# Optimization experiments

Hardware: AMD Instinct MI355X
Metric: run time of the kernel (lower is better)

Reference implementation:

```python
import jax, jax.numpy as jnp
import numpy as np

RBF_DIM = 64          # args.radius_emb_dim
FOLD_DIM = 128        # args.fold_dim
PROT_RADIUS = 30.0    # args.protein_radius (GaussianSmearing stop)
NP_, NL_, E_ = 100000, 50000, 500000


def gaussian_smearing(d):
    # GaussianSmearing(start=0, stop=PROT_RADIUS, num_gaussians=RBF_DIM)
    offsets = jnp.linspace(0.0, PROT_RADIUS, RBF_DIM, dtype=d.dtype)  # [R]
    coeff = -0.5 / (offsets[1] - offsets[0]) ** 2
    return jnp.exp(coeff * (d[:, None] - offsets[None, :]) ** 2)  # [E, R]


def setup_inputs() -> dict:
    key = jax.random.key(0)
    ks = jax.random.split(key, 12)
    scale = 10.0  # spread positions so distances span [0, PROT_RADIUS]
    pos = lambda k, n: jax.random.normal(k, (n, 3), jnp.float32) * scale
    inp = {
        'lig_pos': pos(ks[0], NL_),
        'prot_pos': pos(ks[1], NP_),
        'prot_pos_Cb': pos(ks[2], NP_),
        'prot_pos_C': pos(ks[3], NP_),
        'prot_pos_O': pos(ks[4], NP_),
        'prot_pos_N': pos(ks[5], NP_),
        'W1': jax.random.normal(ks[6], (5 * RBF_DIM, FOLD_DIM), jnp.float32) * 0.05,
        'b1': jnp.zeros((FOLD_DIM,), jnp.float32),
        'W2': jax.random.normal(ks[7], (FOLD_DIM, FOLD_DIM), jnp.float32) * 0.05,
        'b2': jnp.zeros((FOLD_DIM,), jnp.float32),
        'src': jax.random.randint(ks[8], (E_,), 0, NL_, jnp.int32),   # ligand index per edge
        'dst': jax.random.randint(ks[9], (E_,), 0, NP_, jnp.int32),   # protein index per edge
    }
    return inp


def reference(lig_pos, prot_pos, prot_pos_Cb, prot_pos_C, prot_pos_O, prot_pos_N,
              W1, b1, W2, b2, src, dst):
    lp = lig_pos[src]  # [E, 3] gather of ligand positions
    # 5 distance channels: CA/Cb/C/O/N protein atoms, each RBF-smeared
    feats = [gaussian_smearing(jnp.linalg.norm(lp - p[dst], axis=-1))
             for p in (prot_pos, prot_pos_Cb, prot_pos_C, prot_pos_O, prot_pos_N)]
    edge_attr = jnp.concatenate(feats, axis=-1)  # [E, 5*RBF_DIM]
    h = jax.nn.relu(edge_attr @ W1 + b1)         # [E, FOLD_DIM]
    return h @ W2 + b2                           # [E, FOLD_DIM]
```

## Files before the change

kernel.cpp:

```cpp
#include <hip/hip_runtime.h>
#include <hip/hip_bf16.h>

typedef unsigned short ushort_t;
typedef unsigned int uint_t;
typedef __attribute__((ext_vector_type(8))) short short8;
typedef __attribute__((ext_vector_type(4))) float f32x4;
typedef __attribute__((ext_vector_type(2))) uint_t uint2_t;

#define FOLD 128
#define S_CONST 1.78357580f
#define DS_CONST 0.84932180f

__device__ __forceinline__ ushort_t f2bf(float f) {
    uint_t x = __builtin_bit_cast(uint_t, f);
    x += 0x7FFFu + ((x >> 16) & 1u);
    return (ushort_t)(x >> 16);
}

__device__ __forceinline__ uint_t pkbf(float a, float b) {
    __hip_bfloat162 h2 = __float22bfloat162_rn(float2{a, b});
    uint_t u;
    __builtin_memcpy(&u, &h2, sizeof(u));
    return u;
}

__device__ __forceinline__ void softbar() {
    asm volatile("s_waitcnt lgkmcnt(0)" ::: "memory");
    __builtin_amdgcn_s_barrier();
    asm volatile("" ::: "memory");
}

__global__ __launch_bounds__(256) void pack_w(const float* __restrict__ W1,
                                              const float* __restrict__ W2,
                                              ushort_t* __restrict__ W1p,
                                              ushort_t* __restrict__ W2p) {
    int i = blockIdx.x * 256 + threadIdx.x;
    if (i < 40960) {
        int j = i & 7, l = (i >> 3) & 63, nt = (i >> 9) & 7, ks = i >> 12;
        int row = ks * 32 + ((l >> 4) << 3) + j;
        int col = nt * 16 + (l & 15);
        W1p[i] = f2bf(W1[row * FOLD + col]);
    } else if (i < 40960 + 16384) {
        int q = i - 40960;
        int j = q & 7, l = (q >> 3) & 63, nt = (q >> 9) & 7, ks = q >> 12;
        int row = ks * 32 + ((l >> 4) << 3) + j;
        int col = nt * 16 + (l & 15);
        W2p[q] = f2bf(W2[row * FOLD + col]);
    }
}

#define TEDGE 32

__global__ __launch_bounds__(512, 4) void fused(
    const float* __restrict__ lig,
    const float* __restrict__ p0, const float* __restrict__ p1,
    const float* __restrict__ p2, const float* __restrict__ p3,
    const float* __restrict__ p4,
    const ushort_t* __restrict__ W1p, const ushort_t* __restrict__ W2p,
    const float* __restrict__ b1, const float* __restrict__ b2,
    const int* __restrict__ src, const int* __restrict__ dst,
    float* __restrict__ out, int E)
{
    __shared__ float d_lds[2][5][TEDGE];
    __shared__ alignas(16) uint_t attrU[TEDGE * 160];
    __shared__ alignas(16) uint_t h_u[TEDGE * 64];

    const int t = threadIdx.x;
    const int w = t >> 6;
    const int l = t & 63;
    const int lrow = l & 15, lgrp = l >> 4;
    const int aswz = (lrow & 7) << 2;
    const int ntiles = (E + TEDGE - 1) / TEDGE;
    const int G = gridDim.x;

    const short8* W1v = reinterpret_cast<const short8*>(W1p);
    const short8* W2v = reinterpret_cast<const short8*>(W2p);
    short8 wb1[10], wb2[4];
    #pragma unroll
    for (int ks = 0; ks < 10; ++ks) wb1[ks] = W1v[(ks * 8 + w) * 64 + l];
    #pragma unroll
    for (int ks = 0; ks < 4; ++ks)  wb2[ks] = W2v[(ks * 8 + w) * 64 + l];
    f32x4 hb1 = *reinterpret_cast<const f32x4*>(&b1[w * 16 + lgrp * 4]);
    f32x4 hb2 = *reinterpret_cast<const f32x4*>(&b2[w * 16 + lgrp * 4]);

    const bool gth = (t < 160);
    const int g1c = t >> 5, g1m = t & 31;
    const float* GP = (g1c == 0) ? p0 : (g1c == 1) ? p1 : (g1c == 2) ? p2 : (g1c == 3) ? p3 : p4;

    const int m2 = t >> 4, q2 = t & 15;
    const int swz = (m2 & 7) << 2;
    const float ubase = (float)(4 * q2) * DS_CONST;

    int tile = blockIdx.x;
    if (tile >= ntiles) return;

    if (gth) {
        int e = tile * TEDGE + g1m; if (e >= E) e = E - 1;
        int s = src[e], dd = dst[e];
        float dx = lig[3 * s]     - GP[3 * dd];
        float dy = lig[3 * s + 1] - GP[3 * dd + 1];
        float dz = lig[3 * s + 2] - GP[3 * dd + 2];
        d_lds[0][g1c][g1m] = sqrtf(dx * dx + dy * dy + dz * dz);
    }
    int sN = 0, dN = 0;
    if (gth && tile + G < ntiles) {
        int e = (tile + G) * TEDGE + g1m; if (e >= E) e = E - 1;
        sN = src[e]; dN = dst[e];
    }
    softbar();

    int buf = 0;
    while (true) {
        const int next = tile + G;
        const bool havenext = (next < ntiles);

        float ax, ay, az, bx, by, bz;
        if (gth && havenext) {
            ax = lig[3 * sN];     bx = GP[3 * dN];
            ay = lig[3 * sN + 1]; by = GP[3 * dN + 1];
            az = lig[3 * sN + 2]; bz = GP[3 * dN + 2];
        }
        int sN2 = sN, dN2 = dN;
        if (gth && next + G < ntiles) {
            int e = (next + G) * TEDGE + g1m; if (e >= E) e = E - 1;
            sN2 = src[e]; dN2 = dst[e];
        }

        {
            float dv[5];
            #pragma unroll
            for (int c = 0; c < 5; ++c) dv[c] = d_lds[buf][c][m2];
            #pragma unroll
            for (int c = 0; c < 5; ++c) {
                float u0 = __builtin_fmaf(dv[c], S_CONST, -ubase);
                float u1 = u0 - DS_CONST;
                float u2 = u0 - 2.0f * DS_CONST;
                float u3 = u0 - 3.0f * DS_CONST;
                float v0 = __builtin_amdgcn_exp2f(-(u0 * u0));
                float v1 = __builtin_amdgcn_exp2f(-(u1 * u1));
                float v2 = __builtin_amdgcn_exp2f(-(u2 * u2));
                float v3 = __builtin_amdgcn_exp2f(-(u3 * u3));
                uint2_t pv;
                pv[0] = pkbf(v0, v1);
                pv[1] = pkbf(v2, v3);
                int o = 32 * c + 2 * q2;
                *reinterpret_cast<uint2_t*>(&attrU[m2 * 160 + (o ^ swz)]) = pv;
            }
        }
        softbar();

        f32x4 g1[2] = {{0.f,0.f,0.f,0.f},{0.f,0.f,0.f,0.f}};
        #pragma unroll
        for (int ks = 0; ks < 10; ++ks) {
            int o = ks * 16 + lgrp * 4;
            short8 af0 = *reinterpret_cast<const short8*>(&attrU[lrow * 160 + (o ^ aswz)]);
            short8 af1 = *reinterpret_cast<const short8*>(&attrU[(lrow + 16) * 160 + (o ^ aswz)]);
            g1[0] = __builtin_amdgcn_mfma_f32_16x16x32_bf16(wb1[ks], af0, g1[0], 0, 0, 0);
            g1[1] = __builtin_amdgcn_mfma_f32_16x16x32_bf16(wb1[ks], af1, g1[1], 0, 0, 0);
        }

        #pragma unroll
        for (int eh = 0; eh < 2; ++eh) {
            float v0 = fmaxf(g1[eh][0] + hb1[0], 0.f);
            float v1 = fmaxf(g1[eh][1] + hb1[1], 0.f);
            float v2 = fmaxf(g1[eh][2] + hb1[2], 0.f);
            float v3 = fmaxf(g1[eh][3] + hb1[3], 0.f);
            uint2_t pv;
            pv[0] = pkbf(v0, v1);
            pv[1] = pkbf(v2, v3);
            int e = eh * 16 + lrow;
            int dw = (w * 8 + lgrp * 2) ^ ((e & 7) << 2);
            *reinterpret_cast<uint2_t*>(&h_u[e * 64 + dw]) = pv;
        }

        if (gth && havenext) {
            float dx = ax - bx, dy = ay - by, dz = az - bz;
            d_lds[buf ^ 1][g1c][g1m] = sqrtf(dx * dx + dy * dy + dz * dz);
        }
        sN = sN2; dN = dN2;
        softbar();

        f32x4 o2[2] = {{0.f,0.f,0.f,0.f},{0.f,0.f,0.f,0.f}};
        #pragma unroll
        for (int ks = 0; ks < 4; ++ks) {
            int dw = ks * 16 + lgrp * 4;
            short8 hf0 = *reinterpret_cast<const short8*>(&h_u[lrow * 64 + (dw ^ aswz)]);
            short8 hf1 = *reinterpret_cast<const short8*>(&h_u[(lrow + 16) * 64 + (dw ^ aswz)]);
            o2[0] = __builtin_amdgcn_mfma_f32_16x16x32_bf16(wb2[ks], hf0, o2[0], 0, 0, 0);
            o2[1] = __builtin_amdgcn_mfma_f32_16x16x32_bf16(wb2[ks], hf1, o2[1], 0, 0, 0);
        }

        const int e0i = tile * TEDGE;
        #pragma unroll
        for (int eh = 0; eh < 2; ++eh) {
            int e = e0i + eh * 16 + lrow;
            if (e < E) {
                f32x4 v = o2[eh] + hb2;
                __builtin_nontemporal_store(v,
                    reinterpret_cast<f32x4*>(&out[(size_t)e * FOLD + w * 16 + lgrp * 4]));
            }
        }

        if (!havenext) break;
        tile = next;
        buf ^= 1;
    }
}

extern "C" void kernel_launch(void* const* d_in, const int* in_sizes, int n_in,
                              void* d_out, int out_size, void* d_ws, size_t ws_size,
                              hipStream_t stream) {
    const float* lig = (const float*)d_in[0];
    const float* p0  = (const float*)d_in[1];
    const float* p1  = (const float*)d_in[2];
    const float* p2  = (const float*)d_in[3];
    const float* p3  = (const float*)d_in[4];
    const float* p4  = (const float*)d_in[5];
    const float* W1  = (const float*)d_in[6];
    const float* b1  = (const float*)d_in[7];
    const float* W2  = (const float*)d_in[8];
    const float* b2  = (const float*)d_in[9];
    const int* src   = (const int*)d_in[10];
    const int* dst   = (const int*)d_in[11];
    float* out = (float*)d_out;
    const int E = in_sizes[10];

    ushort_t* W1p = (ushort_t*)d_ws;
    ushort_t* W2p = W1p + 40960;

    pack_w<<<(40960 + 16384 + 255) / 256, 256, 0, stream>>>(W1, W2, W1p, W2p);

    int tiles = (E + TEDGE - 1) / TEDGE;
    int nblk = tiles < 512 ? tiles : 512;
    fused<<<nblk, 512, 0, stream>>>(lig, p0, p1, p2, p3, p4, W1p, W2p,
                                    b1, b2, src, dst, out, E);
}
```

Baseline: 110.3 us.

## Drop weight-pack kernel and stage output through LDS for coalesced stores

Removes the separate pack_w launch: each block now reads the fp32 W1/W2 directly and converts them to bf16 MFMA fragments in registers at kernel start. The output tile is first written to a swizzled LDS buffer and then streamed to global memory as contiguous rows per thread, so stores are fully coalesced instead of strided 16-byte fragments. This saves one kernel launch and gives better write coalescing, at the cost of 16KB more LDS per block (which may lower occupancy), an extra barrier per tile, and uncoalesced fp32 weight reads in every block's prologue.

```diff
diff --git a/kernel.cpp b/kernel.cpp
--- a/kernel.cpp
+++ b/kernel.cpp
@@ -11,12 +11,6 @@
 #define S_CONST 1.78357580f
 #define DS_CONST 0.84932180f
 
-__device__ __forceinline__ ushort_t f2bf(float f) {
-    uint_t x = __builtin_bit_cast(uint_t, f);
-    x += 0x7FFFu + ((x >> 16) & 1u);
-    return (ushort_t)(x >> 16);
-}
-
 __device__ __forceinline__ uint_t pkbf(float a, float b) {
     __hip_bfloat162 h2 = __float22bfloat162_rn(float2{a, b});
     uint_t u;
@@ -30,25 +24,6 @@
     asm volatile("" ::: "memory");
 }
 
-__global__ __launch_bounds__(256) void pack_w(const float* __restrict__ W1,
-                                              const float* __restrict__ W2,
-                                              ushort_t* __restrict__ W1p,
-                                              ushort_t* __restrict__ W2p) {
-    int i = blockIdx.x * 256 + threadIdx.x;
-    if (i < 40960) {
-        int j = i & 7, l = (i >> 3) & 63, nt = (i >> 9) & 7, ks = i >> 12;
-        int row = ks * 32 + ((l >> 4) << 3) + j;
-        int col = nt * 16 + (l & 15);
-        W1p[i] = f2bf(W1[row * FOLD + col]);
-    } else if (i < 40960 + 16384) {
-        int q = i - 40960;
-        int j = q & 7, l = (q >> 3) & 63, nt = (q >> 9) & 7, ks = q >> 12;
-        int row = ks * 32 + ((l >> 4) << 3) + j;
-        int col = nt * 16 + (l & 15);
-        W2p[q] = f2bf(W2[row * FOLD + col]);
-    }
-}
-
 #define TEDGE 32
 
 __global__ __launch_bounds__(512, 4) void fused(
@@ -56,7 +31,7 @@
     const float* __restrict__ p0, const float* __restrict__ p1,
     const float* __restrict__ p2, const float* __restrict__ p3,
     const float* __restrict__ p4,
-    const ushort_t* __restrict__ W1p, const ushort_t* __restrict__ W2p,
+    const float* __restrict__ W1, const float* __restrict__ W2,
     const float* __restrict__ b1, const float* __restrict__ b2,
     const int* __restrict__ src, const int* __restrict__ dst,
     float* __restrict__ out, int E)
@@ -64,6 +39,7 @@
     __shared__ float d_lds[2][5][TEDGE];
     __shared__ alignas(16) uint_t attrU[TEDGE * 160];
     __shared__ alignas(16) uint_t h_u[TEDGE * 64];
+    __shared__ alignas(16) float out_s[TEDGE * FOLD];
 
     const int t = threadIdx.x;
     const int w = t >> 6;
@@ -73,13 +49,29 @@
     const int ntiles = (E + TEDGE - 1) / TEDGE;
     const int G = gridDim.x;
 
-    const short8* W1v = reinterpret_cast<const short8*>(W1p);
-    const short8* W2v = reinterpret_cast<const short8*>(W2p);
     short8 wb1[10], wb2[4];
     #pragma unroll
-    for (int ks = 0; ks < 10; ++ks) wb1[ks] = W1v[(ks * 8 + w) * 64 + l];
+    for (int ks = 0; ks < 10; ++ks) {
+        uint_t dwv[4];
+        #pragma unroll
+        for (int jj = 0; jj < 4; ++jj) {
+            float wa = W1[(ks * 32 + lgrp * 8 + 2 * jj)     * FOLD + w * 16 + lrow];
+            float wc = W1[(ks * 32 + lgrp * 8 + 2 * jj + 1) * FOLD + w * 16 + lrow];
+            dwv[jj] = pkbf(wa, wc);
+        }
+        __builtin_memcpy(&wb1[ks], dwv, 16);
+    }
     #pragma unroll
-    for (int ks = 0; ks < 4; ++ks)  wb2[ks] = W2v[(ks * 8 + w) * 64 + l];
+    for (int ks = 0; ks < 4; ++ks) {
+        uint_t dwv[4];
+        #pragma unroll
+        for (int jj = 0; jj < 4; ++jj) {
+            float wa = W2[(ks * 32 + lgrp * 8 + 2 * jj)     * FOLD + w * 16 + lrow];
+            float wc = W2[(ks * 32 + lgrp * 8 + 2 * jj + 1) * FOLD + w * 16 + lrow];
+            dwv[jj] = pkbf(wa, wc);
+        }
+        __builtin_memcpy(&wb2[ks], dwv, 16);
+    }
     f32x4 hb1 = *reinterpret_cast<const f32x4*>(&b1[w * 16 + lgrp * 4]);
     f32x4 hb2 = *reinterpret_cast<const f32x4*>(&b2[w * 16 + lgrp * 4]);
 
@@ -190,14 +182,26 @@
             o2[1] = __builtin_amdgcn_mfma_f32_16x16x32_bf16(wb2[ks], hf1, o2[1], 0, 0, 0);
         }
 
-        const int e0i = tile * TEDGE;
         #pragma unroll
         for (int eh = 0; eh < 2; ++eh) {
-            int e = e0i + eh * 16 + lrow;
-            if (e < E) {
-                f32x4 v = o2[eh] + hb2;
-                __builtin_nontemporal_store(v,
-                    reinterpret_cast<f32x4*>(&out[(size_t)e * FOLD + w * 16 + lgrp * 4]));
+            int e = eh * 16 + lrow;
+            f32x4 v = o2[eh] + hb2;
+            int ch4 = w * 4 + lgrp;
+            *reinterpret_cast<f32x4*>(&out_s[e * FOLD + ((ch4 ^ (e & 7)) << 2)]) = v;
+        }
+        softbar();
+
+        {
+            int e_loc = t >> 4;
+            if (tile * TEDGE + e_loc < E) {
+                float* dp = out + (size_t)tile * TEDGE * FOLD + t * 8;
+                #pragma unroll
+                for (int k = 0; k < 2; ++k) {
+                    int ch4 = (t & 15) * 2 + k;
+                    f32x4 v = *reinterpret_cast<const f32x4*>(
+                        &out_s[e_loc * FOLD + ((ch4 ^ (e_loc & 7)) << 2)]);
+                    __builtin_nontemporal_store(v, reinterpret_cast<f32x4*>(dp) + k);
+                }
             }
         }
 
@@ -225,13 +229,8 @@
     float* out = (float*)d_out;
     const int E = in_sizes[10];
 
-    ushort_t* W1p = (ushort_t*)d_ws;
-    ushort_t* W2p = W1p + 40960;
-
-    pack_w<<<(40960 + 16384 + 255) / 256, 256, 0, stream>>>(W1, W2, W1p, W2p);
-
     int tiles = (E + TEDGE - 1) / TEDGE;
     int nblk = tiles < 512 ? tiles : 512;
-    fused<<<nblk, 512, 0, stream>>>(lig, p0, p1, p2, p3, p4, W1p, W2p,
+    fused<<<nblk, 512, 0, stream>>>(lig, p0, p1, p2, p3, p4, W1, W2,
                                     b1, b2, src, dst, out, E);
 }
```

Result: slower. 123.2 us (+11.6%).
